# Performance work log

Measured on AMD Instinct MI355X. Metric: run time of the kernel, lower is better.

Reference implementation:

```python
import jax, jax.numpy as jnp
import numpy as np

WS = 15
PAD = WS // 2
BN_EPS = 1e-5


def _unfold2d(a, ws):
    # a: (b, t, c, H, W) already padded -> (b, t, c, h, w, ws, ws), stride-1 windows
    h = a.shape[3] - ws + 1
    w = a.shape[4] - ws + 1
    ih = (jnp.arange(h)[:, None] + jnp.arange(ws)[None, :])  # (h, ws)
    iw = (jnp.arange(w)[:, None] + jnp.arange(ws)[None, :])  # (w, ws)
    return a[:, :, :, ih[:, None, :, None], iw[None, :, None, :]]


def setup_inputs() -> dict:
    key = jax.random.key(0)
    ks = jax.random.split(key, 11)
    b, t_mem, c, h, w = 2, 2, 256, 32, 32
    s = 0.05
    return {
        "x": jax.random.normal(ks[0], (b, c, h, w), jnp.float32),
        "mem": jax.random.normal(ks[1], (b, t_mem, c, h, w), jnp.float32),
        "w_qk": jax.random.normal(ks[2], (c // 8, c), jnp.float32) * s,
        "w_qv": jax.random.normal(ks[3], (c // 2, c), jnp.float32) * s,
        "w_mk": jax.random.normal(ks[4], (c // 8, c), jnp.float32) * s,
        "w_mv": jax.random.normal(ks[5], (c // 2, c), jnp.float32) * s,
        "w_smooth": jax.random.normal(ks[6], (c, c), jnp.float32) * s,
        "bn_gamma": jax.random.uniform(ks[7], (c,), jnp.float32, 0.5, 1.5),
        "bn_beta": jax.random.normal(ks[8], (c,), jnp.float32) * 0.1,
        "bn_mean": jnp.zeros((c,), jnp.float32),
        "bn_var": jnp.ones((c,), jnp.float32),
    }


def reference(x, mem, w_qk, w_qv, w_mk, w_mv, w_smooth, bn_gamma, bn_beta, bn_mean, bn_var):
    # mem <- cat([x, mem]) along time: (b, t, c, h, w)
    mem = jnp.concatenate([x[:, None], mem], axis=1)
    b, t, c, h, w = mem.shape

    # 1x1 convs == per-pixel matmuls
    query_k = jnp.einsum('bchw,oc->bohw', x, w_qk)          # (b, c/8, h, w)
    query_v = jnp.einsum('bchw,oc->bohw', x, w_qv)          # (b, c/2, h, w); Dropout2d(p=0) is identity
    mem_k = jnp.einsum('btchw,oc->btohw', mem, w_mk)        # (b, t, c/8, h, w)
    mem_v = jnp.einsum('btchw,oc->btohw', mem, w_mv)        # (b, t, c/2, h, w)

    pad = [(0, 0), (0, 0), (0, 0), (PAD, PAD), (PAD, PAD)]
    unf_k = _unfold2d(jnp.pad(mem_k, pad), WS)              # (b, t, c/8, h, w, ws, ws)
    unf_v = _unfold2d(jnp.pad(mem_v, pad), WS)              # (b, t, c/2, h, w, ws, ws)

    attn = jnp.einsum('bchw,btchwxy->bhwtxy', query_k, unf_k)
    attn = attn.reshape(b, h, w, t * WS * WS)
    # NOTE: faithful to original: softmax over dim=2 (the spatial w axis), not over keys
    attn = jax.nn.softmax(attn, axis=2)

    unf_v = jnp.transpose(unf_v, (0, 2, 3, 4, 1, 5, 6)).reshape(b, c // 2, h, w, t * WS * WS)
    mem_out = jnp.einsum('bhwk,bchwk->bchw', attn, unf_v)   # (b, c/2, h, w)

    feat = jnp.concatenate([query_v, mem_out], axis=1)      # (b, c, h, w)
    y = jnp.einsum('bchw,oc->bohw', feat, w_smooth)
    # BatchNorm2d in eval mode (running stats) + ReLU
    inv = bn_gamma / jnp.sqrt(bn_var + BN_EPS)
    y = y * inv[None, :, None, None] + (bn_beta - bn_mean * inv)[None, :, None, None]
    return jax.nn.relu(y)
```

## Files before the change

kernel.cpp:

```cpp
#include <hip/hip_runtime.h>
#include <math.h>

#define HWSZ 1024
#define HH 32
#define WW 32
#define C 256
#define CK 32
#define CV 128
#define T 3
#define WSZ 15
#define PADSZ 7
#define PADDED 46
#define PP (PADDED*PADDED)
#define KK (T*WSZ*WSZ)
#define B 2
#define NOUT 160
#define KC 32
#define PIXT 32

static const size_t OFF_QK   = 0;
static const size_t OFF_QV   = 65536;
static const size_t OFF_MK   = 327680;
static const size_t OFF_MV   = 733952;
static const size_t OFF_PART = 2359040;

__global__ __launch_bounds__(256) void k_proj(
    const float* __restrict__ x, const float* __restrict__ mem,
    const float* __restrict__ w_qk, const float* __restrict__ w_qv,
    const float* __restrict__ w_mk, const float* __restrict__ w_mv,
    float* __restrict__ ws)
{
    __shared__ float inT[KC][PIXT];
    __shared__ float wT[NOUT][KC + 1];

    int jb   = blockIdx.x >> 5;
    int rowt = blockIdx.x & 31;
    int tid  = threadIdx.x;
    int tx   = tid & 7;
    int ty   = tid >> 3;

    int b, t;
    const float *wk, *wv;
    bool isq;
    if (jb < 6) { b = jb / 3; t = jb % 3; wk = w_mk; wv = w_mv; isq = false; }
    else        { b = jb - 6; t = 0;      wk = w_qk; wv = w_qv; isq = true;  }

    const float* src = (t == 0)
        ? (x + ((size_t)b * C) * HWSZ)
        : (mem + ((size_t)(b * (T - 1) + (t - 1)) * C) * HWSZ);
    int hw0 = rowt * WW;

    float* mk = ws + OFF_MK;
    float* mv = ws + OFF_MV;
    size_t bt = (size_t)(b * T + t);

    if (!isq) {
        int yp = rowt + PADSZ;
        for (int f = tid; f < 448 + 1792; f += 256) {
            if (f < 448) {
                int c = f / 14, sc = f % 14;
                int col = (sc < 7) ? sc : sc + 25;
                mk[(bt * CK + c) * PP + yp * PADDED + col] = 0.f;
            } else {
                int g = f - 448;
                int sc = g >> 7, c = g & 127;
                int col = (sc < 7) ? sc : sc + 25;
                mv[(bt * PP + yp * PADDED + col) * CV + c] = 0.f;
            }
        }
        if (rowt < 14) {
            int pr = (rowt < 7) ? rowt : rowt + 32;
            for (int f = tid; f < 1472 + 5888; f += 256) {
                if (f < 1472) {
                    int c = f / PADDED, col = f % PADDED;
                    mk[(bt * CK + c) * PP + pr * PADDED + col] = 0.f;
                } else {
                    int g = f - 1472;
                    int col = g >> 7, c = g & 127;
                    mv[(bt * PP + pr * PADDED + col) * CV + c] = 0.f;
                }
            }
        }
    }

    float acc[5][4];
    #pragma unroll
    for (int j = 0; j < 5; j++)
        #pragma unroll
        for (int i = 0; i < 4; i++) acc[j][i] = 0.f;

    for (int c0 = 0; c0 < C; c0 += KC) {
        {
            int cc = tid >> 3;
            int p4 = (tid & 7) * 4;
            float4 v = *(const float4*)&src[(size_t)(c0 + cc) * HWSZ + hw0 + p4];
            inT[cc][p4 + 0] = v.x; inT[cc][p4 + 1] = v.y;
            inT[cc][p4 + 2] = v.z; inT[cc][p4 + 3] = v.w;
        }
        #pragma unroll
        for (int j = 0; j < 5; j++) {
            int f  = tid + j * 256;
            int o  = f >> 3;
            int c4 = (f & 7) * 4;
            const float* wr = (o < CK) ? (wk + (size_t)o * C) : (wv + (size_t)(o - CK) * C);
            float4 v = *(const float4*)&wr[c0 + c4];
            wT[o][c4 + 0] = v.x; wT[o][c4 + 1] = v.y;
            wT[o][c4 + 2] = v.z; wT[o][c4 + 3] = v.w;
        }
        __syncthreads();

        #pragma unroll 8
        for (int k = 0; k < KC; k++) {
            float4 iv = *(const float4*)&inT[k][tx * 4];
            #pragma unroll
            for (int j = 0; j < 5; j++) {
                float wv_ = wT[ty * 5 + j][k];
                acc[j][0] += wv_ * iv.x; acc[j][1] += wv_ * iv.y;
                acc[j][2] += wv_ * iv.z; acc[j][3] += wv_ * iv.w;
            }
        }
        __syncthreads();
    }

    int hq = rowt, yp = hq + PADSZ;
    #pragma unroll
    for (int j = 0; j < 5; j++) {
        int o = ty * 5 + j;
        #pragma unroll
        for (int i = 0; i < 4; i++) {
            int wq = tx * 4 + i;
            float v = acc[j][i];
            if (!isq) {
                int xp = wq + PADSZ;
                if (o < CK)
                    mk[(bt * CK + o) * PP + yp * PADDED + xp] = v;
                else
                    mv[(bt * PP + yp * PADDED + xp) * CV + (o - CK)] = v;
            } else {
                int hw = hq * WW + wq;
                if (o < CK) ws[OFF_QK + ((size_t)b * HWSZ + hw) * CK + o] = v;
                else        ws[OFF_QV + ((size_t)(b * CV + (o - CK))) * HWSZ + hw] = v;
            }
        }
    }
}

__global__ __launch_bounds__(256) void k_attn_av(
    const float* __restrict__ qk, const float* __restrict__ mk,
    const float* __restrict__ mv, float* __restrict__ part)
{
    __shared__ float mkl[PADDED][36];
    __shared__ float ql[WW][36];
    __shared__ float V[PADDED][132];
    __shared__ float al[WSZ][WW];

    int blk = blockIdx.x;
    int xg  = blk % 3;
    int rem = blk / 3;
    int t   = rem % T;
    int bh  = rem / T;
    int b   = bh >> 5, hq = bh & 31;
    int tid = threadIdx.x;

    const float* mkb = mk + ((size_t)(b * T + t) * CK) * PP;
    const float* mvb = mv + (size_t)(b * T + t) * PP * CV;

    for (int f = tid; f < WW * CK; f += 256) {
        int w2 = f >> 5, c = f & 31;
        ql[w2][c] = qk[((size_t)(b * HWSZ + hq * WW + w2)) * CK + c];
    }
    __syncthreads();

    int w  = tid & 31;
    int ty = tid >> 5;
    float4 q[8];
    #pragma unroll
    for (int i = 0; i < 8; i++) q[i] = *(const float4*)&ql[w][i * 4];

    int wq = tid & 7, cg = tid >> 3;
    int w0 = wq * 4, c0 = cg * 4;

    float acc[4][4];
    #pragma unroll
    for (int ci = 0; ci < 4; ci++)
        #pragma unroll
        for (int wi = 0; wi < 4; wi++) acc[ci][wi] = 0.f;

    for (int xi = 0; xi < 5; xi++) {
        int xx = xg * 5 + xi;

        for (int f = tid; f < PADDED * 32; f += 256) {
            int col = f >> 5, cq = f & 31;
            float4 v4 = *(const float4*)&mvb[((size_t)(hq + xx) * PADDED + col) * CV + cq * 4];
            V[col][cq * 4 + 0] = v4.x; V[col][cq * 4 + 1] = v4.y;
            V[col][cq * 4 + 2] = v4.z; V[col][cq * 4 + 3] = v4.w;
        }
        for (int f = tid; f < PADDED * CK; f += 256) {
            int c = f / PADDED, col = f - c * PADDED;
            mkl[col][c] = mkb[(size_t)c * PP + (size_t)(hq + xx) * PADDED + col];
        }
        __syncthreads();

        {
            int yy0 = ty, yy1 = ty + 8;
            int row1 = (yy1 < WSZ) ? yy1 : 14;

            float s0 = 0.f, s1 = 0.f;
            #pragma unroll
            for (int cq = 0; cq < 8; cq++) {
                float4 m0 = *(const float4*)&mkl[w + yy0][cq * 4];
                float4 m1 = *(const float4*)&mkl[w + row1][cq * 4];
                s0 += q[cq].x * m0.x + q[cq].y * m0.y + q[cq].z * m0.z + q[cq].w * m0.w;
                s1 += q[cq].x * m1.x + q[cq].y * m1.y + q[cq].z * m1.z + q[cq].w * m1.w;
            }

            float m0 = s0, m1 = s1;
            #pragma unroll
            for (int d = 1; d < 32; d <<= 1) {
                m0 = fmaxf(m0, __shfl_xor(m0, d, 32));
                m1 = fmaxf(m1, __shfl_xor(m1, d, 32));
            }
            float e0 = __expf(s0 - m0), e1 = __expf(s1 - m1);
            float t0 = e0, t1 = e1;
            #pragma unroll
            for (int d = 1; d < 32; d <<= 1) {
                t0 += __shfl_xor(t0, d, 32);
                t1 += __shfl_xor(t1, d, 32);
            }
            al[yy0][w] = e0 / t0;
            if (yy1 < WSZ) al[yy1][w] = e1 / t1;
        }
        __syncthreads();

        {
            float4 vw[18];
            #pragma unroll
            for (int i = 0; i < 18; i++)
                vw[i] = *(const float4*)&V[w0 + i][c0];

            #pragma unroll
            for (int yy = 0; yy < WSZ; yy++) {
                float4 a4 = *(const float4*)&al[yy][w0];
                #pragma unroll
                for (int wi = 0; wi < 4; wi++) {
                    float av = (wi == 0) ? a4.x : (wi == 1) ? a4.y : (wi == 2) ? a4.z : a4.w;
                    float4 vv = vw[yy + wi];
                    acc[0][wi] += av * vv.x;
                    acc[1][wi] += av * vv.y;
                    acc[2][wi] += av * vv.z;
                    acc[3][wi] += av * vv.w;
                }
            }
        }
        __syncthreads();
    }

    float* pbase = part + ((size_t)(bh * 9 + (t * 3 + xg)) * CV) * WW;
    #pragma unroll
    for (int ci = 0; ci < 4; ci++) {
        float4 r; r.x = acc[ci][0]; r.y = acc[ci][1]; r.z = acc[ci][2]; r.w = acc[ci][3];
        *(float4*)&pbase[(c0 + ci) * WW + w0] = r;
    }
}

__global__ __launch_bounds__(256) void k_out(
    const float* __restrict__ qv, const float* __restrict__ part,
    const float* __restrict__ wsm,
    const float* __restrict__ g, const float* __restrict__ bta,
    const float* __restrict__ mean, const float* __restrict__ var,
    float* __restrict__ out)
{
    __shared__ float inT[KC][PIXT];
    __shared__ float wTt[KC][132];

    int blk  = blockIdx.x;
    int oh   = blk & 1;
    int rowt = (blk >> 1) & 31;
    int b    = blk >> 6;
    int tid  = threadIdx.x;
    int tx   = tid & 7;
    int ty   = tid >> 3;
    int hw0  = rowt * WW;
    int obase = oh * 128;
    int bh   = b * HH + rowt;

    float acc[4][4];
    #pragma unroll
    for (int j = 0; j < 4; j++)
        #pragma unroll
        for (int i = 0; i < 4; i++) acc[j][i] = 0.f;

    for (int c0 = 0; c0 < C; c0 += KC) {
        {
            int cc = tid >> 3;
            int p4 = (tid & 7) * 4;
            float4 v;
            if (c0 < CV) {
                v = *(const float4*)&qv[((size_t)(b * CV + c0 + cc)) * HWSZ + hw0 + p4];
            } else {
                int cloc = (c0 - CV) + cc;
                const float* pb = part + ((size_t)bh * 9) * CV * WW + cloc * WW + p4;
                float4 s = *(const float4*)pb;
                #pragma unroll
                for (int tg = 1; tg < 9; tg++) {
                    float4 a = *(const float4*)&pb[(size_t)tg * CV * WW];
                    s.x += a.x; s.y += a.y; s.z += a.z; s.w += a.w;
                }
                v = s;
            }
            inT[cc][p4 + 0] = v.x; inT[cc][p4 + 1] = v.y;
            inT[cc][p4 + 2] = v.z; inT[cc][p4 + 3] = v.w;
        }
        #pragma unroll
        for (int j = 0; j < 4; j++) {
            int f  = tid + j * 256;
            int o  = f >> 3;
            int c4 = (f & 7) * 4;
            float4 v = *(const float4*)&wsm[(size_t)(obase + o) * C + c0 + c4];
            wTt[c4 + 0][o] = v.x; wTt[c4 + 1][o] = v.y;
            wTt[c4 + 2][o] = v.z; wTt[c4 + 3][o] = v.w;
        }
        __syncthreads();

        #pragma unroll 8
        for (int k = 0; k < KC; k++) {
            float4 iv  = *(const float4*)&inT[k][tx * 4];
            float4 wv4 = *(const float4*)&wTt[k][ty * 4];
            acc[0][0] += wv4.x * iv.x; acc[0][1] += wv4.x * iv.y;
            acc[0][2] += wv4.x * iv.z; acc[0][3] += wv4.x * iv.w;
            acc[1][0] += wv4.y * iv.x; acc[1][1] += wv4.y * iv.y;
            acc[1][2] += wv4.y * iv.z; acc[1][3] += wv4.y * iv.w;
            acc[2][0] += wv4.z * iv.x; acc[2][1] += wv4.z * iv.y;
            acc[2][2] += wv4.z * iv.z; acc[2][3] += wv4.z * iv.w;
            acc[3][0] += wv4.w * iv.x; acc[3][1] += wv4.w * iv.y;
            acc[3][2] += wv4.w * iv.z; acc[3][3] += wv4.w * iv.w;
        }
        __syncthreads();
    }

    #pragma unroll
    for (int j = 0; j < 4; j++) {
        int o = obase + ty * 4 + j;
        float inv = g[o] * rsqrtf(var[o] + 1e-5f);
        float sh  = bta[o] - mean[o] * inv;
        float4 r;
        r.x = fmaxf(acc[j][0] * inv + sh, 0.f);
        r.y = fmaxf(acc[j][1] * inv + sh, 0.f);
        r.z = fmaxf(acc[j][2] * inv + sh, 0.f);
        r.w = fmaxf(acc[j][3] * inv + sh, 0.f);
        *(float4*)&out[((size_t)(b * C + o)) * HWSZ + hw0 + tx * 4] = r;
    }
}

extern "C" void kernel_launch(void* const* d_in, const int* in_sizes, int n_in,
                              void* d_out, int out_size, void* d_ws, size_t ws_size,
                              hipStream_t stream) {
    const float* x    = (const float*)d_in[0];
    const float* mem  = (const float*)d_in[1];
    const float* w_qk = (const float*)d_in[2];
    const float* w_qv = (const float*)d_in[3];
    const float* w_mk = (const float*)d_in[4];
    const float* w_mv = (const float*)d_in[5];
    const float* wsm  = (const float*)d_in[6];
    const float* g    = (const float*)d_in[7];
    const float* bta  = (const float*)d_in[8];
    const float* mean = (const float*)d_in[9];
    const float* var  = (const float*)d_in[10];
    float* out = (float*)d_out;
    float* ws  = (float*)d_ws;

    k_proj<<<8 * 32, 256, 0, stream>>>(x, mem, w_qk, w_qv, w_mk, w_mv, ws);
    k_attn_av<<<B * HH * T * 3, 256, 0, stream>>>(ws + OFF_QK, ws + OFF_MK,
                                                  ws + OFF_MV, ws + OFF_PART);
    k_out<<<B * 32 * 2, 256, 0, stream>>>(ws + OFF_QV, ws + OFF_PART, wsm,
                                          g, bta, mean, var, out);
}
```

Before: 105.9 us.

## Store mem_k pixel-major and read K/V directly from global in attention

Changes the mem_k workspace layout from channel-major to pixel-major (channel innermost), so each attention thread can load its key row with contiguous float4 reads. The attention kernel drops its shared-memory staging of K, V and Q, reads them straight from global or cache, and double-buffers the softmax weights so only one barrier per window row is needed. This removes shared-memory traffic and two barriers per iteration. In exchange it depends on L1/L2 for reuse of the overlapping V rows across threads, which may raise global load traffic.

```diff
diff --git a/kernel.cpp b/kernel.cpp
--- a/kernel.cpp
+++ b/kernel.cpp
@@ -58,9 +58,11 @@
         int yp = rowt + PADSZ;
         for (int f = tid; f < 448 + 1792; f += 256) {
             if (f < 448) {
-                int c = f / 14, sc = f % 14;
-                int col = (sc < 7) ? sc : sc + 25;
-                mk[(bt * CK + c) * PP + yp * PADDED + col] = 0.f;
+                int c = f >> 4, sc = f & 15;
+                if (sc < 14) {
+                    int col = (sc < 7) ? sc : sc + 25;
+                    mk[(bt * PP + yp * PADDED + col) * CK + c] = 0.f;
+                }
             } else {
                 int g = f - 448;
                 int sc = g >> 7, c = g & 127;
@@ -72,8 +74,8 @@
             int pr = (rowt < 7) ? rowt : rowt + 32;
             for (int f = tid; f < 1472 + 5888; f += 256) {
                 if (f < 1472) {
-                    int c = f / PADDED, col = f % PADDED;
-                    mk[(bt * CK + c) * PP + pr * PADDED + col] = 0.f;
+                    int col = f >> 5, c = f & 31;
+                    mk[(bt * PP + pr * PADDED + col) * CK + c] = 0.f;
                 } else {
                     int g = f - 1472;
                     int col = g >> 7, c = g & 127;
@@ -133,7 +135,7 @@
             if (!isq) {
                 int xp = wq + PADSZ;
                 if (o < CK)
-                    mk[(bt * CK + o) * PP + yp * PADDED + xp] = v;
+                    mk[(bt * PP + yp * PADDED + xp) * CK + o] = v;
                 else
                     mv[(bt * PP + yp * PADDED + xp) * CV + (o - CK)] = v;
             } else {
@@ -149,10 +151,7 @@
     const float* __restrict__ qk, const float* __restrict__ mk,
     const float* __restrict__ mv, float* __restrict__ part)
 {
-    __shared__ float mkl[PADDED][36];
-    __shared__ float ql[WW][36];
-    __shared__ float V[PADDED][132];
-    __shared__ float al[WSZ][WW];
+    __shared__ float al[2][WSZ][WW];
 
     int blk = blockIdx.x;
     int xg  = blk % 3;
@@ -162,58 +161,56 @@
     int b   = bh >> 5, hq = bh & 31;
     int tid = threadIdx.x;
 
-    const float* mkb = mk + ((size_t)(b * T + t) * CK) * PP;
+    const float* mkb = mk + (size_t)(b * T + t) * PP * CK;
     const float* mvb = mv + (size_t)(b * T + t) * PP * CV;
-
-    for (int f = tid; f < WW * CK; f += 256) {
-        int w2 = f >> 5, c = f & 31;
-        ql[w2][c] = qk[((size_t)(b * HWSZ + hq * WW + w2)) * CK + c];
-    }
-    __syncthreads();
 
     int w  = tid & 31;
     int ty = tid >> 5;
+
     float4 q[8];
-    #pragma unroll
-    for (int i = 0; i < 8; i++) q[i] = *(const float4*)&ql[w][i * 4];
-
-    int wq = tid & 7, cg = tid >> 3;
-    int w0 = wq * 4, c0 = cg * 4;
+    {
+        const float* qrow = qk + ((size_t)(b * HWSZ + hq * WW + w)) * CK;
+        #pragma unroll
+        for (int i = 0; i < 8; i++) q[i] = *(const float4*)&qrow[i * 4];
+    }
+
+    int c0 = w * 4;
+    int w0 = ty * 4;
 
     float acc[4][4];
     #pragma unroll
     for (int ci = 0; ci < 4; ci++)
         #pragma unroll
         for (int wi = 0; wi < 4; wi++) acc[ci][wi] = 0.f;
+
+    int yy0 = ty, yy1r = (ty + 8 < WSZ) ? ty + 8 : WSZ - 1;
+    bool has1 = (ty + 8 < WSZ);
 
     for (int xi = 0; xi < 5; xi++) {
         int xx = xg * 5 + xi;
-
-        for (int f = tid; f < PADDED * 32; f += 256) {
-            int col = f >> 5, cq = f & 31;
-            float4 v4 = *(const float4*)&mvb[((size_t)(hq + xx) * PADDED + col) * CV + cq * 4];
-            V[col][cq * 4 + 0] = v4.x; V[col][cq * 4 + 1] = v4.y;
-            V[col][cq * 4 + 2] = v4.z; V[col][cq * 4 + 3] = v4.w;
-        }
-        for (int f = tid; f < PADDED * CK; f += 256) {
-            int c = f / PADDED, col = f - c * PADDED;
-            mkl[col][c] = mkb[(size_t)c * PP + (size_t)(hq + xx) * PADDED + col];
-        }
-        __syncthreads();
-
+        int buf = xi & 1;
+        const float* mkrow = mkb + (size_t)(hq + xx) * PADDED * CK;
+        const float* vrow  = mvb + (size_t)(hq + xx) * PADDED * CV + c0;
+
+        float s0 = 0.f, s1 = 0.f;
         {
-            int yy0 = ty, yy1 = ty + 8;
-            int row1 = (yy1 < WSZ) ? yy1 : 14;
-
-            float s0 = 0.f, s1 = 0.f;
+            const float* k0 = mkrow + (size_t)(w + yy0) * CK;
+            const float* k1 = mkrow + (size_t)(w + yy1r) * CK;
             #pragma unroll
             for (int cq = 0; cq < 8; cq++) {
-                float4 m0 = *(const float4*)&mkl[w + yy0][cq * 4];
-                float4 m1 = *(const float4*)&mkl[w + row1][cq * 4];
+                float4 m0 = *(const float4*)&k0[cq * 4];
+                float4 m1 = *(const float4*)&k1[cq * 4];
                 s0 += q[cq].x * m0.x + q[cq].y * m0.y + q[cq].z * m0.z + q[cq].w * m0.w;
                 s1 += q[cq].x * m1.x + q[cq].y * m1.y + q[cq].z * m1.z + q[cq].w * m1.w;
             }
-
+        }
+
+        float4 vw[18];
+        #pragma unroll
+        for (int i = 0; i < 18; i++)
+            vw[i] = *(const float4*)&vrow[(size_t)(w0 + i) * CV];
+
+        {
             float m0 = s0, m1 = s1;
             #pragma unroll
             for (int d = 1; d < 32; d <<= 1) {
@@ -227,32 +224,24 @@
                 t0 += __shfl_xor(t0, d, 32);
                 t1 += __shfl_xor(t1, d, 32);
             }
-            al[yy0][w] = e0 / t0;
-            if (yy1 < WSZ) al[yy1][w] = e1 / t1;
-        }
-        __syncthreads();
-
-        {
-            float4 vw[18];
-            #pragma unroll
-            for (int i = 0; i < 18; i++)
-                vw[i] = *(const float4*)&V[w0 + i][c0];
-
-            #pragma unroll
-            for (int yy = 0; yy < WSZ; yy++) {
-                float4 a4 = *(const float4*)&al[yy][w0];
-                #pragma unroll
-                for (int wi = 0; wi < 4; wi++) {
-                    float av = (wi == 0) ? a4.x : (wi == 1) ? a4.y : (wi == 2) ? a4.z : a4.w;
-                    float4 vv = vw[yy + wi];
-                    acc[0][wi] += av * vv.x;
-                    acc[1][wi] += av * vv.y;
-                    acc[2][wi] += av * vv.z;
-                    acc[3][wi] += av * vv.w;
-                }
-            }
-        }
-        __syncthreads();
+            al[buf][yy0][w] = e0 / t0;
+            if (has1) al[buf][yy1r][w] = e1 / t1;
+        }
+        __syncthreads();
+
+        #pragma unroll
+        for (int yy = 0; yy < WSZ; yy++) {
+            float4 a4 = *(const float4*)&al[buf][yy][w0];
+            #pragma unroll
+            for (int wi = 0; wi < 4; wi++) {
+                float av = (wi == 0) ? a4.x : (wi == 1) ? a4.y : (wi == 2) ? a4.z : a4.w;
+                float4 vv = vw[yy + wi];
+                acc[0][wi] += av * vv.x;
+                acc[1][wi] += av * vv.y;
+                acc[2][wi] += av * vv.z;
+                acc[3][wi] += av * vv.w;
+            }
+        }
     }
 
     float* pbase = part + ((size_t)(bh * 9 + (t * 3 + xg)) * CV) * WW;
```

Result: faster. 94.45 us (-10.8%).
